# Performance work log

Hardware: AMD Instinct MI355X
Metric: run time of the kernel (lower is better)

## Reference

```python
import jax, jax.numpy as jnp
import numpy as np

N0, N1, N2 = 400000, 100000, 25000   # nodes per scale (finest -> coarsest)
E0, E1, E2 = 1600000, 400000, 100000
HID, OUT = 64, 2
STATIC_D, DYN_D = 6, 10
K = 3  # filter-matrix polynomial order
NUM_SCALES = 3


def setup_inputs() -> dict:
    key = jax.random.key(0)
    ks = jax.random.split(key, 20)
    def nrm(k, shape, scale=1.0):
        return jax.random.normal(k, shape, dtype=jnp.float32) * scale
    Ntot = N0 + N1 + N2
    inp = {}
    inp["static_features"] = nrm(ks[0], (Ntot, STATIC_D))
    inp["dynamic_features"] = nrm(ks[1], (Ntot, DYN_D))
    Es, Ns = [E0, E1, E2], [N0, N1, N2]
    for i in range(NUM_SCALES):
        inp[f"edge_index{i}"] = jax.random.randint(ks[2 + i], (2, Es[i]), 0, Ns[i], dtype=jnp.int32)
        inp[f"edge_attr{i}"] = jax.random.uniform(ks[5 + i], (Es[i],), dtype=jnp.float32)
    inp["pool_idx1"] = jax.random.randint(ks[8], (N1,), 0, N0, dtype=jnp.int32)
    inp["pool_idx2"] = jax.random.randint(ks[9], (N2,), 0, N0, dtype=jnp.int32)
    fin = STATIC_D + DYN_D
    inp["enc_W1"] = nrm(ks[10], (fin, HID), 1.0 / np.sqrt(fin))
    inp["enc_b1"] = jnp.zeros((HID,), jnp.float32)
    inp["enc_W2"] = nrm(ks[11], (HID, HID), 1.0 / np.sqrt(HID))
    inp["enc_b2"] = jnp.zeros((HID,), jnp.float32)
    inp["enc_prelu"] = jnp.float32(0.25)
    inp["gcn_W"] = nrm(ks[12], (NUM_SCALES, HID, HID), 1.0 / np.sqrt(HID))
    inp["gcn_b"] = jnp.zeros((NUM_SCALES, HID), jnp.float32)
    inp["filter_matrix"] = jnp.ones((NUM_SCALES, K), jnp.float32)
    inp["dec_W1"] = nrm(ks[13], (HID, HID), 1.0 / np.sqrt(HID))
    inp["dec_b1"] = jnp.zeros((HID,), jnp.float32)
    inp["dec_W2"] = nrm(ks[14], (HID, OUT), 1.0 / np.sqrt(HID))
    inp["dec_b2"] = jnp.zeros((OUT,), jnp.float32)
    inp["dec_prelu"] = jnp.float32(0.25)
    return inp


def prelu(x, a):
    return jnp.where(x > 0, x, a * x)


def gcn_conv(x, W, b, src, dst, ew, n):
    # PyG GCNConv: linear, then symmetric-normalized propagation with self loops (weight 1), then bias.
    h = x @ W
    deg = jnp.zeros((n,), x.dtype).at[dst].add(ew) + 1.0  # +1 for self loop
    dinv = jax.lax.rsqrt(deg)
    norm = dinv[src] * ew * dinv[dst]                      # [E]
    out = jnp.zeros_like(h).at[dst].add(norm[:, None] * h[src])
    out = out + h * (dinv * dinv)[:, None]                 # self-loop term: 1/deg
    return out + b


def scatter_mean(x, idx, n):
    cnt = jnp.zeros((n,), x.dtype).at[idx].add(1.0)
    s = jnp.zeros((n, x.shape[1]), x.dtype).at[idx].add(x)
    return s / jnp.maximum(cnt, 1.0)[:, None]


def reference(static_features, dynamic_features, edge_index0, edge_attr0,
              edge_index1, edge_attr1, edge_index2, edge_attr2,
              pool_idx1, pool_idx2,
              enc_W1, enc_b1, enc_W2, enc_b2, enc_prelu,
              gcn_W, gcn_b, filter_matrix,
              dec_W1, dec_b1, dec_W2, dec_b2, dec_prelu):
    # Encoder MLP (prelu after every layer, shared prelu param per MLP)
    x = jnp.concatenate([static_features, dynamic_features], -1)
    x = prelu(x @ enc_W1 + enc_b1, enc_prelu)
    x = prelu(x @ enc_W2 + enc_b2, enc_prelu)

    # Split into scales (node_ptr is static)
    ptr = [0, N0, N0 + N1, N0 + N1 + N2]
    xs = [x[ptr[i]:ptr[i + 1]] for i in range(NUM_SCALES)]
    eis = [edge_index0, edge_index1, edge_index2]
    eas = [edge_attr0, edge_attr1, edge_attr2]
    Ns = [N0, N1, N2]

    # MSGNN layers: K repeated (conv -> tanh), mixed by filter_matrix
    outs = []
    for i in range(NUM_SCALES):
        src, dst = eis[i][0], eis[i][1]
        h = xs[i]
        acc = jnp.zeros_like(h)
        for k in range(K):
            h = jnp.tanh(gcn_conv(h, gcn_W[i], gcn_b[i], src, dst, eas[i], Ns[i]))
            acc = acc + filter_matrix[i, k] * h
        outs.append(acc)

    # Skip-connection pooling: scatter-mean coarse scales onto finest scale
    fin = outs[0]
    fin = fin + scatter_mean(outs[1], pool_idx1, N0)
    fin = fin + scatter_mean(outs[2], pool_idx2, N0)

    # Decoder MLP
    y = prelu(fin @ dec_W1 + dec_b1, dec_prelu)
    y = prelu(y @ dec_W2 + dec_b2, dec_prelu)
    return y
```

## Files before the change

kernel.cpp:

```cpp
#include <hip/hip_runtime.h>
#include <hip/hip_bf16.h>

typedef __hip_bfloat16 bf16;
typedef short  bf16x8  __attribute__((ext_vector_type(8)));
typedef __bf16 bf16x8n __attribute__((ext_vector_type(8)));
typedef float  f32x4   __attribute__((ext_vector_type(4)));
typedef unsigned long long u64;

constexpr int cN0 = 400000, cN1 = 100000, cN2 = 25000;
constexpr int cNTOT = cN0 + cN1 + cN2;
constexpr int cE0 = 1600000, cE1 = 400000, cE2 = 100000;

static __device__ __forceinline__ float b2f(bf16 x) { return __bfloat162float(x); }
static __device__ __forceinline__ float bflo(unsigned u) { return __uint_as_float(u << 16); }
static __device__ __forceinline__ float bfhi(unsigned u) { return __uint_as_float(u & 0xffff0000u); }

static __device__ __forceinline__ short f2bf_rtne(float f) {
    unsigned u = __float_as_uint(f);
    u = (u + 0x7fffu + ((u >> 16) & 1u)) >> 16;
    return (short)u;
}
static __device__ __forceinline__ void split2(float x, short& h, short& l) {
    unsigned u = __float_as_uint(x);
    h = (short)(u >> 16);
    l = f2bf_rtne(x - __uint_as_float(u & 0xffff0000u));
}

static __device__ __forceinline__ f32x4 mfma16(bf16x8 a, bf16x8 b, f32x4 c) {
    return __builtin_amdgcn_mfma_f32_16x16x32_bf16((bf16x8n)a, (bf16x8n)b, c, 0, 0, 0);
}

static __device__ __forceinline__ void pack_a8(const float* s8, bf16x8& ah, bf16x8& al) {
    float4 v0 = ((const float4*)s8)[0];
    float4 v1 = ((const float4*)s8)[1];
    float xx[8] = {v0.x, v0.y, v0.z, v0.w, v1.x, v1.y, v1.z, v1.w};
#pragma unroll
    for (int j = 0; j < 8; j++) { short h, l; split2(xx[j], h, l); ah[j] = h; al[j] = l; }
}

static __device__ __forceinline__ void pack_b8(const float* __restrict__ W, int ldn,
                                               int kbase, int col, int kmax,
                                               bf16x8& bh, bf16x8& bl) {
#pragma unroll
    for (int j = 0; j < 8; j++) {
        int k = kbase + j;
        float w = (k < kmax) ? W[(size_t)k * ldn + col] : 0.f;
        short h, l; split2(w, h, l); bh[j] = h; bl[j] = l;
    }
}

__global__ __launch_bounds__(256, 2)
void enc_kernel(const float* __restrict__ stat, const float* __restrict__ dyn,
                const float* __restrict__ W1, const float* __restrict__ b1,
                const float* __restrict__ W2, const float* __restrict__ b2,
                const float* __restrict__ pa, bf16* __restrict__ X, int nn)
{
    __shared__ float sF[4][16 * 20];
    __shared__ float sH[4][16 * 68];
    const int lane = threadIdx.x & 63;
    const int slot = threadIdx.x >> 6;
    const int r = lane & 15, g4 = lane >> 4;
    const int wid = blockIdx.x * (blockDim.x >> 6) + slot;
    const int nw  = gridDim.x * (blockDim.x >> 6);

    bf16x8 B1h[4], B1l[4], B2h[2][4], B2l[2][4];
#pragma unroll
    for (int nb = 0; nb < 4; nb++)
        pack_b8(W1, 64, g4 * 8, nb * 16 + r, 16, B1h[nb], B1l[nb]);
#pragma unroll
    for (int s = 0; s < 2; s++)
#pragma unroll
        for (int nb = 0; nb < 4; nb++)
            pack_b8(W2, 64, s * 32 + g4 * 8, nb * 16 + r, 64, B2h[s][nb], B2l[s][nb]);
    float bc1[4], bc2[4];
#pragma unroll
    for (int nb = 0; nb < 4; nb++) { bc1[nb] = b1[nb * 16 + r]; bc2[nb] = b2[nb * 16 + r]; }
    const float a = pa[0];
    float* F = sF[slot];
    float* H = sH[slot];
    const int ntile = (nn + 15) >> 4;

    for (int tt = wid; tt < ntile; tt += nw) {
        const int n0 = tt << 4;
        const int nv = min(16, nn - n0);
        for (int t = lane; t < nv * 6; t += 64)
            F[(t / 6) * 20 + (t % 6)] = stat[(size_t)n0 * 6 + t];
        for (int t = lane; t < nv * 10; t += 64)
            F[(t / 10) * 20 + 6 + (t % 10)] = dyn[(size_t)n0 * 10 + t];
        __builtin_amdgcn_wave_barrier();

        f32x4 C1[4];
#pragma unroll
        for (int nb = 0; nb < 4; nb++) C1[nb] = (f32x4){bc1[nb], bc1[nb], bc1[nb], bc1[nb]};
        bf16x8 ah, al;
        if (g4 < 2) pack_a8(F + r * 20 + g4 * 8, ah, al);
        else        { ah = (bf16x8)(short)0; al = (bf16x8)(short)0; }
#pragma unroll
        for (int nb = 0; nb < 4; nb++) {
            C1[nb] = mfma16(ah, B1h[nb], C1[nb]);
            C1[nb] = mfma16(ah, B1l[nb], C1[nb]);
            C1[nb] = mfma16(al, B1h[nb], C1[nb]);
        }
#pragma unroll
        for (int nb = 0; nb < 4; nb++)
#pragma unroll
            for (int q = 0; q < 4; q++) {
                float v = C1[nb][q];
                v = v > 0.f ? v : a * v;
                H[(g4 * 4 + q) * 68 + nb * 16 + r] = v;
            }
        __builtin_amdgcn_wave_barrier();

        f32x4 C2[4];
#pragma unroll
        for (int nb = 0; nb < 4; nb++) C2[nb] = (f32x4){bc2[nb], bc2[nb], bc2[nb], bc2[nb]};
#pragma unroll
        for (int s = 0; s < 2; s++) {
            bf16x8 a2h, a2l;
            pack_a8(H + r * 68 + s * 32 + g4 * 8, a2h, a2l);
#pragma unroll
            for (int nb = 0; nb < 4; nb++) {
                C2[nb] = mfma16(a2h, B2h[s][nb], C2[nb]);
                C2[nb] = mfma16(a2h, B2l[s][nb], C2[nb]);
                C2[nb] = mfma16(a2l, B2h[s][nb], C2[nb]);
            }
        }
#pragma unroll
        for (int nb = 0; nb < 4; nb++)
#pragma unroll
            for (int q = 0; q < 4; q++) {
                float v = C2[nb][q];
                v = v > 0.f ? v : a * v;
                const int row = g4 * 4 + q;
                if (row < nv)
                    X[(size_t)(n0 + row) * 64 + nb * 16 + r] = __float2bfloat16(v);
            }
        __builtin_amdgcn_wave_barrier();
    }
}

__global__ void zdc_kernel(u64* p, int n)
{
    int t = blockIdx.x * 256 + threadIdx.x;
    if (t < n) p[t] = 0ull;
}
__global__ void edge_pack_kernel(const int* __restrict__ dst, const float* __restrict__ ew,
                                 u64* __restrict__ dc, int ne)
{
    int e = blockIdx.x * 256 + threadIdx.x;
    if (e < ne) {
        u64 pk = (1ull << 40) | (u64)(ew[e] * 268435456.f + 0.5f);
        atomicAdd(&dc[dst[e]], pk);
    }
}

__global__ void scan_blk_kernel(const u64* __restrict__ dc, int* __restrict__ base,
                                int* __restrict__ bsum, float* __restrict__ dinv, int n)
{
    __shared__ int s[256];
    const int tid = threadIdx.x;
    const int t = blockIdx.x * 256 + tid;
    u64 pk = (t < n) ? dc[t] : 0ull;
    int v = (int)(pk >> 40);
    s[tid] = v;
    __syncthreads();
#pragma unroll
    for (int d = 1; d < 256; d <<= 1) {
        int u = (tid >= d) ? s[tid - d] : 0;
        __syncthreads();
        s[tid] += u;
        __syncthreads();
    }
    if (t < n) {
        base[t] = s[tid] - v;
        const float deg = 1.f + (float)(pk & ((1ull << 40) - 1ull)) * (1.f / 268435456.f);
        dinv[t] = rsqrtf(deg);
    }
    if (tid == 255) bsum[blockIdx.x] = s[255];
}
__global__ void scan_top_kernel(int* __restrict__ bsum, int nb)
{
    __shared__ int s[256];
    __shared__ int carry;
    const int tid = threadIdx.x;
    if (tid == 0) carry = 0;
    __syncthreads();
    for (int c0 = 0; c0 < nb; c0 += 256) {
        const int t = c0 + tid;
        int v = (t < nb) ? bsum[t] : 0;
        s[tid] = v;
        __syncthreads();
#pragma unroll
        for (int d = 1; d < 256; d <<= 1) {
            int u = (tid >= d) ? s[tid - d] : 0;
            __syncthreads();
            s[tid] += u;
            __syncthreads();
        }
        if (t < nb) bsum[t] = carry + s[tid] - v;
        __syncthreads();
        if (tid == 255) carry += s[255];
        __syncthreads();
    }
}
__global__ void scan_add_kernel(int* __restrict__ base, const int* __restrict__ bsum,
                                int* __restrict__ cur, int n)
{
    const int t = blockIdx.x * 256 + threadIdx.x;
    if (t < n) { int b = base[t] + bsum[blockIdx.x]; base[t] = b; cur[t] = b; }
}

__global__ void grab_kernel(const int* __restrict__ cnt, int* __restrict__ base,
                            int* __restrict__ cur, int* __restrict__ gc, int n)
{
    int t = blockIdx.x * 256 + threadIdx.x;
    if (t < n) { int b = atomicAdd(gc, cnt[t]); base[t] = b; cur[t] = b; }
}
__global__ void fill_edge_kernel(const int* __restrict__ src, const int* __restrict__ dst,
                                 const float* __restrict__ ew, const float* __restrict__ dinv,
                                 int* __restrict__ cur, int* __restrict__ srcp,
                                 bf16* __restrict__ normp, int ne)
{
    int e = blockIdx.x * 256 + threadIdx.x;
    if (e >= ne) return;
    int d = dst[e], s = src[e];
    int pos = atomicAdd(&cur[d], 1);
    srcp[pos]  = s;
    normp[pos] = __float2bfloat16(dinv[s] * ew[e] * dinv[d]);
}
__global__ void zint2_kernel(int* __restrict__ p, int* __restrict__ gc, int n)
{
    int t = blockIdx.x * 256 + threadIdx.x;
    if (t < n) p[t] = 0;
    if (t == 0) gc[0] = 0;
}
__global__ void cnt_idx_kernel(const int* __restrict__ idx, int* __restrict__ cnt, int n)
{
    int j = blockIdx.x * 256 + threadIdx.x;
    if (j < n) atomicAdd(&cnt[idx[j]], 1);
}
__global__ void fill_idx_kernel(const int* __restrict__ idx, int* __restrict__ cur,
                                int* __restrict__ jp, int n)
{
    int j = blockIdx.x * 256 + threadIdx.x;
    if (j >= n) return;
    int pos = atomicAdd(&cur[idx[j]], 1);
    jp[pos] = j;
}

__global__ __launch_bounds__(256, 4)
void fused_conv_kernel(const int* __restrict__ base,
                       const int* __restrict__ srcp, const bf16* __restrict__ normp,
                       const bf16* __restrict__ h_in, bf16* __restrict__ h_out,
                       const float* __restrict__ dinv,
                       const float* __restrict__ W, int woff,
                       const float* __restrict__ bias, int boff,
                       const float* __restrict__ filt, int foff,
                       int first, int store_h, float* __restrict__ acc,
                       int nn, int ne)
{
    __shared__ float sb[4][16 * 68];
    __shared__ unsigned sW[64 * 65];
    const int lane = threadIdx.x & 63;
    const int slot = threadIdx.x >> 6;
    const int r = lane & 15, g4 = lane >> 4;
    const int wid  = blockIdx.x * (blockDim.x >> 6) + slot;
    const int nw   = gridDim.x * (blockDim.x >> 6);

    if (slot == 0) {
        unsigned* dstw = sW + lane * 65;
#pragma unroll
        for (int s = 0; s < 2; s++)
#pragma unroll
            for (int nb = 0; nb < 4; nb++) {
                bf16x8 bh, bl;
                pack_b8(W + woff, 64, s * 32 + g4 * 8, nb * 16 + r, 64, bh, bl);
                const int f = s * 4 + nb;
                uint4 uh = *(uint4*)&bh;
                uint4 ul = *(uint4*)&bl;
                dstw[f * 4 + 0] = uh.x; dstw[f * 4 + 1] = uh.y;
                dstw[f * 4 + 2] = uh.z; dstw[f * 4 + 3] = uh.w;
                dstw[32 + f * 4 + 0] = ul.x; dstw[32 + f * 4 + 1] = ul.y;
                dstw[32 + f * 4 + 2] = ul.z; dstw[32 + f * 4 + 3] = ul.w;
            }
    }
    __syncthreads();

    float bc[4];
#pragma unroll
    for (int nb = 0; nb < 4; nb++) bc[nb] = bias[boff + nb * 16 + r];
    const float fc = filt[foff];
    float* sbrow = sb[slot];
    const unsigned* myW = sW + lane * 65;
    const int ngrp = (nn + 15) >> 4;

    for (int grp = wid; grp < ngrp; grp += nw) {
        const int n0 = grp << 4;
        int rpl = 0;
        if (lane <= 16) rpl = (n0 + lane < nn) ? base[n0 + lane] : ne;
        const int b4 = g4 << 2;
        const int q0 = __shfl(rpl, b4);
        const int q1 = __shfl(rpl, b4 + 1);
        const int q2 = __shfl(rpl, b4 + 2);
        const int q3 = __shfl(rpl, b4 + 3);
        const int q4 = __shfl(rpl, b4 + 4);

        int   curl  = 0;
        int   rnext = q1;
        float g0 = 0.f, g1 = 0.f, g2 = 0.f, g3 = 0.f;
        auto flush = [&]() {
            *(float4*)(sbrow + (b4 + curl) * 68 + (r << 2)) = make_float4(g0, g1, g2, g3);
            g0 = g1 = g2 = g3 = 0.f;
            curl++;
            rnext = (curl == 1) ? q2 : (curl == 2) ? q3 : (curl == 3) ? q4 : 0x7fffffff;
        };

        for (int eb = q0; eb < q4; eb += 16) {
            const int ei_ = min(eb + r, q4 - 1);
            int   sv = srcp[ei_];
            float nv = (eb + r < q4) ? b2f(normp[ei_]) : 0.f;
#pragma unroll
            for (int t = 0; t < 16; t += 8) {
                const int bidx = (g4 << 4) + t;
                int ss[8]; float mm[8]; uint2 pp[8];
#pragma unroll
                for (int j = 0; j < 8; j++) {
                    ss[j] = __shfl(sv, bidx + j);
                    mm[j] = __shfl(nv, bidx + j);
                }
#pragma unroll
                for (int j = 0; j < 8; j++)
                    pp[j] = *(const uint2*)(h_in + ((size_t)ss[j] << 6) + (r << 2));
#pragma unroll
                for (int j = 0; j < 8; j++) {
                    while (eb + t + j >= rnext) flush();
                    g0 += mm[j] * bflo(pp[j].x); g1 += mm[j] * bfhi(pp[j].x);
                    g2 += mm[j] * bflo(pp[j].y); g3 += mm[j] * bfhi(pp[j].y);
                }
            }
        }
        while (curl < 4) flush();
        __builtin_amdgcn_wave_barrier();

        {
            const int node = n0 + r;
            const int ncl = min(node, nn - 1);
            float di = dinv[ncl];
            di = (node < nn) ? di * di : 0.f;
            float* rowp = sbrow + r * 68 + (g4 << 4);
#pragma unroll
            for (int hh = 0; hh < 2; hh++) {
                uint4 hv = *(const uint4*)(h_in + ((size_t)ncl << 6) + (g4 << 4) + hh * 8);
                float4 f0 = *(float4*)(rowp + hh * 8);
                float4 f1 = *(float4*)(rowp + hh * 8 + 4);
                f0.x += di * bflo(hv.x); f0.y += di * bfhi(hv.x);
                f0.z += di * bflo(hv.y); f0.w += di * bfhi(hv.y);
                f1.x += di * bflo(hv.z); f1.y += di * bfhi(hv.z);
                f1.z += di * bflo(hv.w); f1.w += di * bfhi(hv.w);
                *(float4*)(rowp + hh * 8)     = f0;
                *(float4*)(rowp + hh * 8 + 4) = f1;
            }
        }
        __builtin_amdgcn_wave_barrier();

        const int nv16 = min(16, nn - n0);
        f32x4 C[4];
#pragma unroll
        for (int nb = 0; nb < 4; nb++) C[nb] = (f32x4){bc[nb], bc[nb], bc[nb], bc[nb]};
#pragma unroll
        for (int s = 0; s < 2; s++) {
            bf16x8 ah, al;
            pack_a8(sbrow + r * 68 + s * 32 + g4 * 8, ah, al);
#pragma unroll
            for (int nb = 0; nb < 4; nb++) {
                const int f = s * 4 + nb;
                uint4 uh = *(const uint4*)(myW + f * 4);
                uint4 ul = *(const uint4*)(myW + 32 + f * 4);
                bf16x8 bh = *(bf16x8*)&uh;
                bf16x8 bl = *(bf16x8*)&ul;
                C[nb] = mfma16(ah, bh, C[nb]);
                C[nb] = mfma16(ah, bl, C[nb]);
                C[nb] = mfma16(al, bh, C[nb]);
            }
        }
#pragma unroll
        for (int nb = 0; nb < 4; nb++)
#pragma unroll
            for (int q = 0; q < 4; q++) {
                const int row = g4 * 4 + q;
                if (row < nv16) {
                    const float sv_ = C[nb][q];
                    const float e = __expf(2.f * sv_);
                    const float h = 1.f - 2.f * __builtin_amdgcn_rcpf(e + 1.f);
                    const size_t ai = (size_t)(n0 + row) * 64 + nb * 16 + r;
                    if (store_h) h_out[ai] = __float2bfloat16(h);
                    acc[ai] = (first ? 0.f : acc[ai]) + fc * h;
                }
            }
        __builtin_amdgcn_wave_barrier();
    }
}

__global__ void pool_gather_kernel(const int* __restrict__ base, const int* __restrict__ cnt,
                                   const int* __restrict__ jp, const float* __restrict__ accc,
                                   float* __restrict__ fin, int nn)
{
    const int lane = threadIdx.x & 63;
    const int n = blockIdx.x * (blockDim.x >> 6) + (threadIdx.x >> 6);
    if (n >= nn) return;
    const int m = cnt[n];
    if (m == 0) return;
    const int bs = base[n];
    float s = 0.f;
    for (int t = bs; t < bs + m; t++) {
        int j = jp[t];
        s += accc[(size_t)j * 64 + lane];
    }
    fin[(size_t)n * 64 + lane] += s / (float)m;
}

__global__ __launch_bounds__(256, 3)
void dec_kernel(const float* __restrict__ fin,
                const float* __restrict__ W1, const float* __restrict__ b1,
                const float* __restrict__ W2, const float* __restrict__ b2,
                const float* __restrict__ pa, float* __restrict__ out, int nn)
{
    const int lane = threadIdx.x & 63;
    const int r = lane & 15, g4 = lane >> 4;
    const int wid = blockIdx.x * (blockDim.x >> 6) + (threadIdx.x >> 6);
    const int nw  = gridDim.x * (blockDim.x >> 6);

    bf16x8 Wh[2][4], Wl[2][4];
#pragma unroll
    for (int s = 0; s < 2; s++)
#pragma unroll
        for (int nb = 0; nb < 4; nb++)
            pack_b8(W1, 64, s * 32 + g4 * 8, nb * 16 + r, 64, Wh[s][nb], Wl[s][nb]);
    float bc[4], w20[4], w21[4];
#pragma unroll
    for (int nb = 0; nb < 4; nb++) {
        bc[nb]  = b1[nb * 16 + r];
        w20[nb] = W2[(nb * 16 + r) * 2 + 0];
        w21[nb] = W2[(nb * 16 + r) * 2 + 1];
    }
    const float bb20 = b2[0], bb21 = b2[1];
    const float a = pa[0];
    const int ntile = (nn + 15) >> 4;

    for (int tt = wid; tt < ntile; tt += nw) {
        const int n0 = tt << 4;
        f32x4 C[4];
#pragma unroll
        for (int nb = 0; nb < 4; nb++) C[nb] = (f32x4){bc[nb], bc[nb], bc[nb], bc[nb]};
#pragma unroll
        for (int s = 0; s < 2; s++) {
            bf16x8 ah, al;
            pack_a8(fin + (size_t)(n0 + r) * 64 + s * 32 + g4 * 8, ah, al);
#pragma unroll
            for (int nb = 0; nb < 4; nb++) {
                C[nb] = mfma16(ah, Wh[s][nb], C[nb]);
                C[nb] = mfma16(ah, Wl[s][nb], C[nb]);
                C[nb] = mfma16(al, Wh[s][nb], C[nb]);
            }
        }
#pragma unroll
        for (int q = 0; q < 4; q++) {
            float p0 = 0.f, p1 = 0.f;
#pragma unroll
            for (int nb = 0; nb < 4; nb++) {
                float y = C[nb][q];
                y = y > 0.f ? y : a * y;
                p0 += y * w20[nb]; p1 += y * w21[nb];
            }
            p0 += __shfl_xor(p0, 1); p1 += __shfl_xor(p1, 1);
            p0 += __shfl_xor(p0, 2); p1 += __shfl_xor(p1, 2);
            p0 += __shfl_xor(p0, 4); p1 += __shfl_xor(p1, 4);
            p0 += __shfl_xor(p0, 8); p1 += __shfl_xor(p1, 8);
            if (r == 0) {
                const int node = n0 + g4 * 4 + q;
                if (node < nn) {
                    float o0 = p0 + bb20; o0 = o0 > 0.f ? o0 : a * o0;
                    float o1 = p1 + bb21; o1 = o1 > 0.f ? o1 : a * o1;
                    ((float2*)out)[node] = make_float2(o0, o1);
                }
            }
        }
    }
}

extern "C" void kernel_launch(void* const* d_in, const int* in_sizes, int n_in,
                              void* d_out, int out_size, void* d_ws, size_t ws_size,
                              hipStream_t stream)
{
    const float* stat = (const float*)d_in[0];
    const float* dyn  = (const float*)d_in[1];
    const int*   ei[3]   = {(const int*)d_in[2], (const int*)d_in[4], (const int*)d_in[6]};
    const float* ea[3]   = {(const float*)d_in[3], (const float*)d_in[5], (const float*)d_in[7]};
    const int*   pidx[2] = {(const int*)d_in[8], (const int*)d_in[9]};
    const float* encW1 = (const float*)d_in[10]; const float* encb1 = (const float*)d_in[11];
    const float* encW2 = (const float*)d_in[12]; const float* encb2 = (const float*)d_in[13];
    const float* encpa = (const float*)d_in[14];
    const float* gW    = (const float*)d_in[15]; const float* gbias = (const float*)d_in[16];
    const float* filt  = (const float*)d_in[17];
    const float* dW1   = (const float*)d_in[18]; const float* db1   = (const float*)d_in[19];
    const float* dW2   = (const float*)d_in[20]; const float* db2   = (const float*)d_in[21];
    const float* dpa   = (const float*)d_in[22];

    auto al = [](size_t x) { return (x + 255) & ~(size_t)255; };
    char* w = (char*)d_ws;
    size_t off = 0;
    bf16* X    = (bf16*)(w + off); off += al((size_t)cNTOT * 64 * 2);
    bf16* HB   = (bf16*)(w + off); off += al((size_t)cN0 * 64 * 2);
    float* FIN = (float*)(w + off); off += al((size_t)cN0 * 64 * 4);
    float* ACCC= (float*)(w + off); off += al((size_t)cN1 * 64 * 4);
    float* DINV= (float*)(w + off); off += al((size_t)cN0 * 4);
    int* CNTI  = (int*)(w + off);  off += al((size_t)cN0 * 4);
    int* BASE  = (int*)(w + off);  off += al((size_t)cN0 * 4);
    int* CUR   = (int*)(w + off);  off += al((size_t)cN0 * 4);
    int* SRCP  = (int*)(w + off);  off += al((size_t)cE0 * 4);
    bf16* NORMP= (bf16*)(w + off); off += al((size_t)cE0 * 2);
    int* JP    = (int*)(w + off);  off += al((size_t)cN1 * 4);
    int* GC    = (int*)(w + off);  off += 256;
    int* BSUM  = (int*)(w + off);  off += al((size_t)2048 * 4);
    u64* DC    = (u64*)ACCC;

    const int Ns[3]  = {cN0, cN1, cN2};
    const int Es[3]  = {cE0, cE1, cE2};
    const int ptr[3] = {0, cN0, cN0 + cN1};
#define NB(x) (((x) + 255) / 256)

    enc_kernel<<<4096, 256, 0, stream>>>(stat, dyn, encW1, encb1, encW2, encb2, encpa, X, cNTOT);

    for (int i = 0; i < 3; i++) {
        const int* srcp_in = ei[i];
        const int* dstp    = ei[i] + Es[i];
        zdc_kernel      <<<NB(Ns[i]), 256, 0, stream>>>(DC, Ns[i]);
        edge_pack_kernel<<<NB(Es[i]), 256, 0, stream>>>(dstp, ea[i], DC, Es[i]);
        scan_blk_kernel <<<NB(Ns[i]), 256, 0, stream>>>(DC, BASE, BSUM, DINV, Ns[i]);
        scan_top_kernel <<<1, 256, 0, stream>>>(BSUM, NB(Ns[i]));
        scan_add_kernel <<<NB(Ns[i]), 256, 0, stream>>>(BASE, BSUM, CUR, Ns[i]);
        fill_edge_kernel<<<NB(Es[i]), 256, 0, stream>>>(srcp_in, dstp, ea[i], DINV, CUR, SRCP, NORMP, Es[i]);

        bf16* ping = X + (size_t)ptr[i] * 64;
        bf16* pong = HB;
        float* acc_i = (i == 0) ? FIN : ACCC;
        const int ngrp = (Ns[i] + 15) / 16;
        const int cblk = max(1, min(4096, (ngrp + 3) / 4));
        for (int k = 0; k < 3; k++) {
            bf16* hin  = (k & 1) ? pong : ping;
            bf16* hout = (k & 1) ? ping : pong;
            fused_conv_kernel<<<cblk, 256, 0, stream>>>(BASE, SRCP, NORMP,
                hin, hout, DINV, gW, i * 4096, gbias, i * 64,
                filt, i * 3 + k, (k == 0) ? 1 : 0, (k < 2) ? 1 : 0, acc_i, Ns[i], Es[i]);
        }
        if (i >= 1) {
            int nj = (i == 1) ? cN1 : cN2;
            const int* pp = pidx[i - 1];
            zint2_kernel   <<<NB(cN0), 256, 0, stream>>>(CNTI, GC, cN0);
            cnt_idx_kernel <<<NB(nj), 256, 0, stream>>>(pp, CNTI, nj);
            grab_kernel    <<<NB(cN0), 256, 0, stream>>>(CNTI, BASE, CUR, GC, cN0);
            fill_idx_kernel<<<NB(nj), 256, 0, stream>>>(pp, CUR, JP, nj);
            pool_gather_kernel<<<(cN0 + 3) / 4, 256, 0, stream>>>(BASE, CNTI, JP, ACCC, FIN, cN0);
        }
    }
    dec_kernel<<<4096, 256, 0, stream>>>(FIN, dW1, db1, dW2, db2, dpa, (float*)d_out, cN0);
#undef NB
}
```

Baseline: 1.260 ms.

## Fuse decoder MLP into final finest-scale conv and reorder scales to coarse-first

Processes coarse scales first so pooled contributions are written into FIN before the finest scale runs, then fuses the final finest-scale GCN conv with the decoder MLP in one kernel. This removes the separate decoder pass, which re-read the full FIN buffer, and avoids storing the last h and acc values. The first pool pass now overwrites FIN instead of accumulating, so no zero-init is needed. The fused kernel uses more LDS and registers, which may reduce occupancy.

```diff
diff --git a/kernel.cpp b/kernel.cpp
--- a/kernel.cpp
+++ b/kernel.cpp
@@ -47,6 +47,26 @@
         float w = (k < kmax) ? W[(size_t)k * ldn + col] : 0.f;
         short h, l; split2(w, h, l); bh[j] = h; bl[j] = l;
     }
+}
+
+static __device__ __forceinline__ void pack_w_lds(const float* __restrict__ W,
+                                                  unsigned* __restrict__ sw,
+                                                  int lane, int r, int g4) {
+    unsigned* dstw = sw + lane * 65;
+#pragma unroll
+    for (int s = 0; s < 2; s++)
+#pragma unroll
+        for (int nb = 0; nb < 4; nb++) {
+            bf16x8 bh, bl;
+            pack_b8(W, 64, s * 32 + g4 * 8, nb * 16 + r, 64, bh, bl);
+            const int f = s * 4 + nb;
+            uint4 uh = *(uint4*)&bh;
+            uint4 ul = *(uint4*)&bl;
+            dstw[f * 4 + 0] = uh.x; dstw[f * 4 + 1] = uh.y;
+            dstw[f * 4 + 2] = uh.z; dstw[f * 4 + 3] = uh.w;
+            dstw[32 + f * 4 + 0] = ul.x; dstw[32 + f * 4 + 1] = ul.y;
+            dstw[32 + f * 4 + 2] = ul.z; dstw[32 + f * 4 + 3] = ul.w;
+        }
 }
 
 __global__ __launch_bounds__(256, 2)
@@ -267,23 +287,7 @@
     const int wid  = blockIdx.x * (blockDim.x >> 6) + slot;
     const int nw   = gridDim.x * (blockDim.x >> 6);
 
-    if (slot == 0) {
-        unsigned* dstw = sW + lane * 65;
-#pragma unroll
-        for (int s = 0; s < 2; s++)
-#pragma unroll
-            for (int nb = 0; nb < 4; nb++) {
-                bf16x8 bh, bl;
-                pack_b8(W + woff, 64, s * 32 + g4 * 8, nb * 16 + r, 64, bh, bl);
-                const int f = s * 4 + nb;
-                uint4 uh = *(uint4*)&bh;
-                uint4 ul = *(uint4*)&bl;
-                dstw[f * 4 + 0] = uh.x; dstw[f * 4 + 1] = uh.y;
-                dstw[f * 4 + 2] = uh.z; dstw[f * 4 + 3] = uh.w;
-                dstw[32 + f * 4 + 0] = ul.x; dstw[32 + f * 4 + 1] = ul.y;
-                dstw[32 + f * 4 + 2] = ul.z; dstw[32 + f * 4 + 3] = ul.w;
-            }
-    }
+    if (slot == 0) pack_w_lds(W + woff, sW, lane, r, g4);
     __syncthreads();
 
     float bc[4];
@@ -401,66 +405,172 @@
     }
 }
 
-__global__ void pool_gather_kernel(const int* __restrict__ base, const int* __restrict__ cnt,
-                                   const int* __restrict__ jp, const float* __restrict__ accc,
-                                   float* __restrict__ fin, int nn)
-{
+__global__ __launch_bounds__(256, 4)
+void fused_conv_dec_kernel(const int* __restrict__ base,
+                           const int* __restrict__ srcp, const bf16* __restrict__ normp,
+                           const bf16* __restrict__ h_in,
+                           const float* __restrict__ dinv,
+                           const float* __restrict__ W, int woff,
+                           const float* __restrict__ bias, int boff,
+                           const float* __restrict__ filt, int foff,
+                           const float* __restrict__ acc,
+                           const float* __restrict__ dW1, const float* __restrict__ db1,
+                           const float* __restrict__ dW2, const float* __restrict__ db2,
+                           const float* __restrict__ dpa,
+                           float* __restrict__ out, int nn, int ne)
+{
+    __shared__ float sb[4][16 * 68];
+    __shared__ unsigned sW[64 * 65];
+    __shared__ unsigned sWd[64 * 65];
     const int lane = threadIdx.x & 63;
-    const int n = blockIdx.x * (blockDim.x >> 6) + (threadIdx.x >> 6);
-    if (n >= nn) return;
-    const int m = cnt[n];
-    if (m == 0) return;
-    const int bs = base[n];
-    float s = 0.f;
-    for (int t = bs; t < bs + m; t++) {
-        int j = jp[t];
-        s += accc[(size_t)j * 64 + lane];
-    }
-    fin[(size_t)n * 64 + lane] += s / (float)m;
-}
-
-__global__ __launch_bounds__(256, 3)
-void dec_kernel(const float* __restrict__ fin,
-                const float* __restrict__ W1, const float* __restrict__ b1,
-                const float* __restrict__ W2, const float* __restrict__ b2,
-                const float* __restrict__ pa, float* __restrict__ out, int nn)
-{
-    const int lane = threadIdx.x & 63;
+    const int slot = threadIdx.x >> 6;
     const int r = lane & 15, g4 = lane >> 4;
-    const int wid = blockIdx.x * (blockDim.x >> 6) + (threadIdx.x >> 6);
-    const int nw  = gridDim.x * (blockDim.x >> 6);
-
-    bf16x8 Wh[2][4], Wl[2][4];
-#pragma unroll
-    for (int s = 0; s < 2; s++)
-#pragma unroll
-        for (int nb = 0; nb < 4; nb++)
-            pack_b8(W1, 64, s * 32 + g4 * 8, nb * 16 + r, 64, Wh[s][nb], Wl[s][nb]);
-    float bc[4], w20[4], w21[4];
+    const int wid  = blockIdx.x * (blockDim.x >> 6) + slot;
+    const int nw   = gridDim.x * (blockDim.x >> 6);
+
+    if (slot == 0) pack_w_lds(W + woff, sW, lane, r, g4);
+    if (slot == 1) pack_w_lds(dW1, sWd, lane, r, g4);
+    __syncthreads();
+
+    float bc[4], bcd[4], w20[4], w21[4];
 #pragma unroll
     for (int nb = 0; nb < 4; nb++) {
-        bc[nb]  = b1[nb * 16 + r];
-        w20[nb] = W2[(nb * 16 + r) * 2 + 0];
-        w21[nb] = W2[(nb * 16 + r) * 2 + 1];
-    }
-    const float bb20 = b2[0], bb21 = b2[1];
-    const float a = pa[0];
-    const int ntile = (nn + 15) >> 4;
-
-    for (int tt = wid; tt < ntile; tt += nw) {
-        const int n0 = tt << 4;
+        bc[nb]  = bias[boff + nb * 16 + r];
+        bcd[nb] = db1[nb * 16 + r];
+        w20[nb] = dW2[(nb * 16 + r) * 2 + 0];
+        w21[nb] = dW2[(nb * 16 + r) * 2 + 1];
+    }
+    const float fc = filt[foff];
+    const float bb20 = db2[0], bb21 = db2[1];
+    const float ad = dpa[0];
+    float* sbrow = sb[slot];
+    const unsigned* myW  = sW  + lane * 65;
+    const unsigned* myWd = sWd + lane * 65;
+    const int ngrp = (nn + 15) >> 4;
+
+    for (int grp = wid; grp < ngrp; grp += nw) {
+        const int n0 = grp << 4;
+        int rpl = 0;
+        if (lane <= 16) rpl = (n0 + lane < nn) ? base[n0 + lane] : ne;
+        const int b4 = g4 << 2;
+        const int q0 = __shfl(rpl, b4);
+        const int q1 = __shfl(rpl, b4 + 1);
+        const int q2 = __shfl(rpl, b4 + 2);
+        const int q3 = __shfl(rpl, b4 + 3);
+        const int q4 = __shfl(rpl, b4 + 4);
+
+        int   curl  = 0;
+        int   rnext = q1;
+        float g0 = 0.f, g1 = 0.f, g2 = 0.f, g3 = 0.f;
+        auto flush = [&]() {
+            *(float4*)(sbrow + (b4 + curl) * 68 + (r << 2)) = make_float4(g0, g1, g2, g3);
+            g0 = g1 = g2 = g3 = 0.f;
+            curl++;
+            rnext = (curl == 1) ? q2 : (curl == 2) ? q3 : (curl == 3) ? q4 : 0x7fffffff;
+        };
+
+        for (int eb = q0; eb < q4; eb += 16) {
+            const int ei_ = min(eb + r, q4 - 1);
+            int   sv = srcp[ei_];
+            float nv = (eb + r < q4) ? b2f(normp[ei_]) : 0.f;
+#pragma unroll
+            for (int t = 0; t < 16; t += 8) {
+                const int bidx = (g4 << 4) + t;
+                int ss[8]; float mm[8]; uint2 pp[8];
+#pragma unroll
+                for (int j = 0; j < 8; j++) {
+                    ss[j] = __shfl(sv, bidx + j);
+                    mm[j] = __shfl(nv, bidx + j);
+                }
+#pragma unroll
+                for (int j = 0; j < 8; j++)
+                    pp[j] = *(const uint2*)(h_in + ((size_t)ss[j] << 6) + (r << 2));
+#pragma unroll
+                for (int j = 0; j < 8; j++) {
+                    while (eb + t + j >= rnext) flush();
+                    g0 += mm[j] * bflo(pp[j].x); g1 += mm[j] * bfhi(pp[j].x);
+                    g2 += mm[j] * bflo(pp[j].y); g3 += mm[j] * bfhi(pp[j].y);
+                }
+            }
+        }
+        while (curl < 4) flush();
+        __builtin_amdgcn_wave_barrier();
+
+        {
+            const int node = n0 + r;
+            const int ncl = min(node, nn - 1);
+            float di = dinv[ncl];
+            di = (node < nn) ? di * di : 0.f;
+            float* rowp = sbrow + r * 68 + (g4 << 4);
+#pragma unroll
+            for (int hh = 0; hh < 2; hh++) {
+                uint4 hv = *(const uint4*)(h_in + ((size_t)ncl << 6) + (g4 << 4) + hh * 8);
+                float4 f0 = *(float4*)(rowp + hh * 8);
+                float4 f1 = *(float4*)(rowp + hh * 8 + 4);
+                f0.x += di * bflo(hv.x); f0.y += di * bfhi(hv.x);
+                f0.z += di * bflo(hv.y); f0.w += di * bfhi(hv.y);
+                f1.x += di * bflo(hv.z); f1.y += di * bfhi(hv.z);
+                f1.z += di * bflo(hv.w); f1.w += di * bfhi(hv.w);
+                *(float4*)(rowp + hh * 8)     = f0;
+                *(float4*)(rowp + hh * 8 + 4) = f1;
+            }
+        }
+        __builtin_amdgcn_wave_barrier();
+
+        const int nv16 = min(16, nn - n0);
         f32x4 C[4];
 #pragma unroll
         for (int nb = 0; nb < 4; nb++) C[nb] = (f32x4){bc[nb], bc[nb], bc[nb], bc[nb]};
 #pragma unroll
         for (int s = 0; s < 2; s++) {
             bf16x8 ah, al;
-            pack_a8(fin + (size_t)(n0 + r) * 64 + s * 32 + g4 * 8, ah, al);
+            pack_a8(sbrow + r * 68 + s * 32 + g4 * 8, ah, al);
 #pragma unroll
             for (int nb = 0; nb < 4; nb++) {
-                C[nb] = mfma16(ah, Wh[s][nb], C[nb]);
-                C[nb] = mfma16(ah, Wl[s][nb], C[nb]);
-                C[nb] = mfma16(al, Wh[s][nb], C[nb]);
+                const int f = s * 4 + nb;
+                uint4 uh = *(const uint4*)(myW + f * 4);
+                uint4 ul = *(const uint4*)(myW + 32 + f * 4);
+                bf16x8 bh = *(bf16x8*)&uh;
+                bf16x8 bl = *(bf16x8*)&ul;
+                C[nb] = mfma16(ah, bh, C[nb]);
+                C[nb] = mfma16(ah, bl, C[nb]);
+                C[nb] = mfma16(al, bh, C[nb]);
+            }
+        }
+        __builtin_amdgcn_wave_barrier();
+
+#pragma unroll
+        for (int nb = 0; nb < 4; nb++)
+#pragma unroll
+            for (int q = 0; q < 4; q++) {
+                const int row = g4 * 4 + q;
+                float y = 0.f;
+                if (row < nv16) {
+                    const float e = __expf(2.f * C[nb][q]);
+                    const float h = 1.f - 2.f * __builtin_amdgcn_rcpf(e + 1.f);
+                    y = acc[(size_t)(n0 + row) * 64 + nb * 16 + r] + fc * h;
+                }
+                sbrow[row * 68 + nb * 16 + r] = y;
+            }
+        __builtin_amdgcn_wave_barrier();
+
+        f32x4 D[4];
+#pragma unroll
+        for (int nb = 0; nb < 4; nb++) D[nb] = (f32x4){bcd[nb], bcd[nb], bcd[nb], bcd[nb]};
+#pragma unroll
+        for (int s = 0; s < 2; s++) {
+            bf16x8 ah, al;
+            pack_a8(sbrow + r * 68 + s * 32 + g4 * 8, ah, al);
+#pragma unroll
+            for (int nb = 0; nb < 4; nb++) {
+                const int f = s * 4 + nb;
+                uint4 uh = *(const uint4*)(myWd + f * 4);
+                uint4 ul = *(const uint4*)(myWd + 32 + f * 4);
+                bf16x8 bh = *(bf16x8*)&uh;
+                bf16x8 bl = *(bf16x8*)&ul;
+                D[nb] = mfma16(ah, bh, D[nb]);
+                D[nb] = mfma16(ah, bl, D[nb]);
+                D[nb] = mfma16(al, bh, D[nb]);
             }
         }
 #pragma unroll
@@ -468,9 +578,9 @@
             float p0 = 0.f, p1 = 0.f;
 #pragma unroll
             for (int nb = 0; nb < 4; nb++) {
-                float y = C[nb][q];
-                y = y > 0.f ? y : a * y;
-                p0 += y * w20[nb]; p1 += y * w21[nb];
+                float yv = D[nb][q];
+                yv = yv > 0.f ? yv : ad * yv;
+                p0 += yv * w20[nb]; p1 += yv * w21[nb];
             }
             p0 += __shfl_xor(p0, 1); p1 += __shfl_xor(p1, 1);
             p0 += __shfl_xor(p0, 2); p1 += __shfl_xor(p1, 2);
@@ -479,13 +589,34 @@
             if (r == 0) {
                 const int node = n0 + g4 * 4 + q;
                 if (node < nn) {
-                    float o0 = p0 + bb20; o0 = o0 > 0.f ? o0 : a * o0;
-                    float o1 = p1 + bb21; o1 = o1 > 0.f ? o1 : a * o1;
+                    float o0 = p0 + bb20; o0 = o0 > 0.f ? o0 : ad * o0;
+                    float o1 = p1 + bb21; o1 = o1 > 0.f ? o1 : ad * o1;
                     ((float2*)out)[node] = make_float2(o0, o1);
                 }
             }
         }
-    }
+        __builtin_amdgcn_wave_barrier();
+    }
+}
+
+__global__ void pool_gather_kernel(const int* __restrict__ base, const int* __restrict__ cnt,
+                                   const int* __restrict__ jp, const float* __restrict__ accc,
+                                   float* __restrict__ fin, int nn, int firstw)
+{
+    const int lane = threadIdx.x & 63;
+    const int n = blockIdx.x * (blockDim.x >> 6) + (threadIdx.x >> 6);
+    if (n >= nn) return;
+    const int m = cnt[n];
+    if (!firstw && m == 0) return;
+    const int bs = base[n];
+    float s = 0.f;
+    for (int t = bs; t < bs + m; t++) {
+        int j = jp[t];
+        s += accc[(size_t)j * 64 + lane];
+    }
+    const float v = m ? s / (float)m : 0.f;
+    if (firstw) fin[(size_t)n * 64 + lane] = v;
+    else        fin[(size_t)n * 64 + lane] += v;
 }
 
 extern "C" void kernel_launch(void* const* d_in, const int* in_sizes, int n_in,
@@ -527,11 +658,13 @@
     const int Ns[3]  = {cN0, cN1, cN2};
     const int Es[3]  = {cE0, cE1, cE2};
     const int ptr[3] = {0, cN0, cN0 + cN1};
+    const int order[3] = {1, 2, 0};
 #define NB(x) (((x) + 255) / 256)
 
     enc_kernel<<<4096, 256, 0, stream>>>(stat, dyn, encW1, encb1, encW2, encb2, encpa, X, cNTOT);
 
-    for (int i = 0; i < 3; i++) {
+    for (int oi = 0; oi < 3; oi++) {
+        const int i = order[oi];
         const int* srcp_in = ei[i];
         const int* dstp    = ei[i] + Es[i];
         zdc_kernel      <<<NB(Ns[i]), 256, 0, stream>>>(DC, Ns[i]);
@@ -549,9 +682,16 @@
         for (int k = 0; k < 3; k++) {
             bf16* hin  = (k & 1) ? pong : ping;
             bf16* hout = (k & 1) ? ping : pong;
-            fused_conv_kernel<<<cblk, 256, 0, stream>>>(BASE, SRCP, NORMP,
-                hin, hout, DINV, gW, i * 4096, gbias, i * 64,
-                filt, i * 3 + k, (k == 0) ? 1 : 0, (k < 2) ? 1 : 0, acc_i, Ns[i], Es[i]);
+            if (i == 0 && k == 2) {
+                fused_conv_dec_kernel<<<cblk, 256, 0, stream>>>(BASE, SRCP, NORMP,
+                    hin, DINV, gW, 0, gbias, 0, filt, 2, FIN,
+                    dW1, db1, dW2, db2, dpa, (float*)d_out, Ns[0], Es[0]);
+            } else {
+                const int first = (i == 0) ? 0 : (k == 0 ? 1 : 0);
+                fused_conv_kernel<<<cblk, 256, 0, stream>>>(BASE, SRCP, NORMP,
+                    hin, hout, DINV, gW, i * 4096, gbias, i * 64,
+                    filt, i * 3 + k, first, (k < 2) ? 1 : 0, acc_i, Ns[i], Es[i]);
+            }
         }
         if (i >= 1) {
             int nj = (i == 1) ? cN1 : cN2;
@@ -560,9 +700,9 @@
             cnt_idx_kernel <<<NB(nj), 256, 0, stream>>>(pp, CNTI, nj);
             grab_kernel    <<<NB(cN0), 256, 0, stream>>>(CNTI, BASE, CUR, GC, cN0);
             fill_idx_kernel<<<NB(nj), 256, 0, stream>>>(pp, CUR, JP, nj);
-            pool_gather_kernel<<<(cN0 + 3) / 4, 256, 0, stream>>>(BASE, CNTI, JP, ACCC, FIN, cN0);
-        }
-    }
-    dec_kernel<<<4096, 256, 0, stream>>>(FIN, dW1, db1, dW2, db2, dpa, (float*)d_out, cN0);
+            pool_gather_kernel<<<(cN0 + 3) / 4, 256, 0, stream>>>(BASE, CNTI, JP, ACCC, FIN,
+                                                                  cN0, (i == 1) ? 1 : 0);
+        }
+    }
 #undef NB
 }
```

Result: slower. 1.319 ms (+4.7%).
